# Performance work log

Hardware: AMD Instinct MI355X
Metric: run time of the kernel (lower is better)

The kernel has to match this reference:

```python
import jax, jax.numpy as jnp
import numpy as np

N, E, C = 50000, 800000, 128
NEG_SLOPE = 0.01

def leaky(v):
    return jnp.where(v >= 0, v, NEG_SLOPE * v)

def setup_inputs() -> dict:
    key = jax.random.key(0)
    ks = jax.random.split(key, 16)
    s = lambda *sh: 1.0 / np.sqrt(sh[0])
    return {
        "x": jax.random.normal(ks[0], (N, C), dtype=jnp.float32),
        "pos": jax.random.normal(ks[1], (N, 3), dtype=jnp.float32),
        "edge_index": jax.random.randint(ks[2], (2, E), 0, N, dtype=jnp.int64),
        # mlp_h: Linear(C,C) -> LeakyReLU -> Linear(C,3) -> Tanh
        "h_w1": jax.random.uniform(ks[3], (C, C), jnp.float32, -s(C), s(C)),
        "h_b1": jax.random.uniform(ks[4], (C,), jnp.float32, -s(C), s(C)),
        "h_w2": jax.random.uniform(ks[5], (C, 3), jnp.float32, -s(C), s(C)),
        "h_b2": jax.random.uniform(ks[6], (3,), jnp.float32, -s(C), s(C)),
        # mlp_f: Linear(C+3, C) -> LeakyReLU
        "f_w": jax.random.uniform(ks[7], (C + 3, C), jnp.float32, -s(C + 3), s(C + 3)),
        "f_b": jax.random.uniform(ks[8], (C,), jnp.float32, -s(C + 3), s(C + 3)),
        # mlp_g: Linear(C,C) -> LeakyReLU -> Linear(C,C)
        "g_w1": jax.random.uniform(ks[9], (C, C), jnp.float32, -s(C), s(C)),
        "g_b1": jax.random.uniform(ks[10], (C,), jnp.float32, -s(C), s(C)),
        "g_w2": jax.random.uniform(ks[11], (C, C), jnp.float32, -s(C), s(C)),
        "g_b2": jax.random.uniform(ks[12], (C,), jnp.float32, -s(C), s(C)),
    }

def reference(x, pos, edge_index, h_w1, h_b1, h_w2, h_b2, f_w, f_b,
              g_w1, g_b1, g_w2, g_b2):
    src = edge_index[0]  # j (source)
    dst = edge_index[1]  # i (target)
    # delta_i = mlp_h(x_i): [N, 3]
    delta = jnp.tanh(leaky(x @ h_w1 + h_b1) @ h_w2 + h_b2)
    # edge message: mlp_f(cat([pos_j - pos_i + delta_i, x_j]))  -> [E, C]
    rel = pos[src] - pos[dst] + delta[dst]            # [E, 3]
    msg_in = jnp.concatenate([rel, x[src]], axis=-1)  # [E, C+3]
    e = leaky(msg_in @ f_w + f_b)                     # [E, C]
    # sum-aggregate messages at target nodes
    aggr = jax.ops.segment_sum(e, dst, num_segments=N)  # [N, C]
    # out = mlp_g(aggr) + x
    out = leaky(aggr @ g_w1 + g_b1) @ g_w2 + g_b2 + x
    return out
```

## Files before the change

### kernel.cpp

```cpp
#include <hip/hip_runtime.h>
#include <hip/hip_bf16.h>
#include <math.h>


typedef __attribute__((ext_vector_type(8))) short bf16x8;
typedef __attribute__((ext_vector_type(4))) float f32x4;

#define LEAKY(v) ((v) >= 0.0f ? (v) : 0.01f * (v))

#define KMAX 512
#define S3_BATCH 8192
#define AGG_CAP 16384

static __device__ __forceinline__ unsigned short f2bf(float f) {
    unsigned u = __float_as_uint(f);
    u = (u + 0x7fffu + ((u >> 16) & 1u)) >> 16;
    return (unsigned short)u;
}

union ABu { unsigned short u[8]; bf16x8 v; };

static __device__ __forceinline__ bf16x8 cvt8(const float* __restrict__ p) {
    ABu r;
    const float4 v0 = *(const float4*)p;
    const float4 v1 = *(const float4*)(p + 4);
    r.u[0] = f2bf(v0.x); r.u[1] = f2bf(v0.y); r.u[2] = f2bf(v0.z); r.u[3] = f2bf(v0.w);
    r.u[4] = f2bf(v1.x); r.u[5] = f2bf(v1.y); r.u[6] = f2bf(v1.z); r.u[7] = f2bf(v1.w);
    return r.v;
}

static __device__ __forceinline__ bf16x8 zero_ab() {
    ABu r;
    #pragma unroll
    for (int i = 0; i < 8; ++i) r.u[i] = 0;
    return r.v;
}

static __device__ __forceinline__ void stage_weight(
    const unsigned short* __restrict__ src, unsigned short (*dst)[136], int tid)
{
    #pragma unroll
    for (int it = 0; it < 8; ++it) {
        const int c   = it * 256 + tid;
        const int row = c >> 4;
        const int col = (c & 15) * 8;
        *(uint4*)&dst[row][col] = *(const uint4*)(src + row * 128 + col);
    }
}

__global__ __launch_bounds__(128) void prep_weights(
    const float* __restrict__ h_w1, const float* __restrict__ f_w,
    const float* __restrict__ g_w1, const float* __restrict__ g_w2,
    unsigned short* __restrict__ Wht, unsigned short* __restrict__ Wft,
    unsigned short* __restrict__ G1t, unsigned short* __restrict__ G2t,
    int* __restrict__ bincnt, int* __restrict__ done)
{
    const int j = blockIdx.x;
    const int k = threadIdx.x;
    if (j == 0) {
        for (int i = k; i < KMAX; i += 128) bincnt[i] = 0;
        if (k == 0) *done = 0;
    }
    Wht[j * 128 + k] = f2bf(h_w1[(size_t)k * 128 + j]);
    Wft[j * 128 + k] = f2bf(f_w[(size_t)(3 + k) * 128 + j]);
    G1t[j * 128 + k] = f2bf(g_w1[(size_t)k * 128 + j]);
    G2t[j * 128 + k] = f2bf(g_w2[(size_t)k * 128 + j]);
}

__global__ __launch_bounds__(256) void node_pre(
    const float* __restrict__ x, const float* __restrict__ pos,
    const unsigned short* __restrict__ Wht, const float* __restrict__ h_b1,
    const float* __restrict__ h_w2, const float* __restrict__ h_b2,
    const unsigned short* __restrict__ Wft, const float* __restrict__ f_b,
    const float* __restrict__ fw3,
    float* __restrict__ deltap, unsigned short* __restrict__ Zb, int N)
{
    __shared__ unsigned short Ws[128][136];
    __shared__ float cb[128][8];

    const int tid  = threadIdx.x;
    const int lane = tid & 63;
    const int wave = tid >> 6;
    const int quad = lane >> 4;
    const int l16  = lane & 15;
    const int row0 = blockIdx.x * 64 + wave * 16;

    if (tid < 128) {
        cb[tid][0] = h_b1[tid];
        cb[tid][1] = f_b[tid];
        cb[tid][2] = h_w2[tid * 3 + 0];
        cb[tid][3] = h_w2[tid * 3 + 1];
        cb[tid][4] = h_w2[tid * 3 + 2];
        cb[tid][5] = fw3[tid];
        cb[tid][6] = fw3[128 + tid];
        cb[tid][7] = fw3[256 + tid];
    }
    stage_weight(Wht, Ws, tid);

    bf16x8 a[4];
    {
        const int row = row0 + l16;
        if (row < N) {
            const float* xp = x + (size_t)row * 128 + quad * 8;
            #pragma unroll
            for (int kc = 0; kc < 4; ++kc) a[kc] = cvt8(xp + kc * 32);
        } else {
            #pragma unroll
            for (int kc = 0; kc < 4; ++kc) a[kc] = zero_ab();
        }
    }

    float px[4], py[4], pz[4];
    #pragma unroll
    for (int reg = 0; reg < 4; ++reg) {
        const int grow = row0 + quad * 4 + reg;
        const int gr = (grow < N) ? grow : 0;
        px[reg] = pos[(size_t)gr * 3 + 0];
        py[reg] = pos[(size_t)gr * 3 + 1];
        pz[reg] = pos[(size_t)gr * 3 + 2];
    }
    __syncthreads();

    f32x4 acch[8];
    #pragma unroll
    for (int nt = 0; nt < 8; ++nt) acch[nt] = (f32x4){0.f, 0.f, 0.f, 0.f};
    #pragma unroll
    for (int nt = 0; nt < 8; ++nt) {
        const unsigned short* wp = &Ws[nt * 16 + l16][quad * 8];
        #pragma unroll
        for (int kc = 0; kc < 4; ++kc) {
            const bf16x8 b = *(const bf16x8*)(wp + kc * 32);
            acch[nt] = __builtin_amdgcn_mfma_f32_16x16x32_bf16(a[kc], b, acch[nt], 0, 0, 0);
        }
    }

    __syncthreads();
    stage_weight(Wft, Ws, tid);
    __syncthreads();

    f32x4 accf[8];
    #pragma unroll
    for (int nt = 0; nt < 8; ++nt) accf[nt] = (f32x4){0.f, 0.f, 0.f, 0.f};
    #pragma unroll
    for (int nt = 0; nt < 8; ++nt) {
        const unsigned short* wp = &Ws[nt * 16 + l16][quad * 8];
        #pragma unroll
        for (int kc = 0; kc < 4; ++kc) {
            const bf16x8 b = *(const bf16x8*)(wp + kc * 32);
            accf[nt] = __builtin_amdgcn_mfma_f32_16x16x32_bf16(a[kc], b, accf[nt], 0, 0, 0);
        }
    }

    float p[4][3];
    #pragma unroll
    for (int r = 0; r < 4; ++r) { p[r][0] = 0.f; p[r][1] = 0.f; p[r][2] = 0.f; }

    #pragma unroll
    for (int nt = 0; nt < 8; ++nt) {
        const int col = nt * 16 + l16;
        const float b1  = cb[col][0];
        const float fb  = cb[col][1];
        const float w20 = cb[col][2];
        const float w21 = cb[col][3];
        const float w22 = cb[col][4];
        const float wxc = cb[col][5];
        const float wyc = cb[col][6];
        const float wzc = cb[col][7];
        #pragma unroll
        for (int reg = 0; reg < 4; ++reg) {
            const int grow = row0 + quad * 4 + reg;
            float h = acch[nt][reg] + b1;
            h = LEAKY(h);
            p[reg][0] += h * w20;
            p[reg][1] += h * w21;
            p[reg][2] += h * w22;
            if (grow < N) {
                const float z = accf[nt][reg] + fb
                              + px[reg] * wxc + py[reg] * wyc + pz[reg] * wzc;
                Zb[(size_t)grow * 128 + col] = f2bf(z);
            }
        }
    }

    #pragma unroll
    for (int reg = 0; reg < 4; ++reg)
        #pragma unroll
        for (int c = 0; c < 3; ++c) {
            float v = p[reg][c];
            v += __shfl_down(v, 8);
            v += __shfl_down(v, 4);
            v += __shfl_down(v, 2);
            v += __shfl_down(v, 1);
            p[reg][c] = v;
        }

    if (l16 == 0) {
        #pragma unroll
        for (int reg = 0; reg < 4; ++reg) {
            const int grow = row0 + quad * 4 + reg;
            if (grow < N) {
                deltap[(size_t)grow * 3 + 0] = tanhf(p[reg][0] + h_b2[0]) - px[reg];
                deltap[(size_t)grow * 3 + 1] = tanhf(p[reg][1] + h_b2[1]) - py[reg];
                deltap[(size_t)grow * 3 + 2] = tanhf(p[reg][2] + h_b2[2]) - pz[reg];
            }
        }
    }
}

__global__ __launch_bounds__(512) void coarse_hist(
    const int* __restrict__ ei, int* __restrict__ bincnt,
    int* __restrict__ binstart, int* __restrict__ cursors,
    int* __restrict__ done, int E, int K)
{
    __shared__ int h[KMAX];
    __shared__ int s[512];
    __shared__ int lastflag;
    const int tid = threadIdx.x;
    for (int k = tid; k < K; k += 512) h[k] = 0;
    __syncthreads();
    const int stride = gridDim.x * 512;
    for (int e = blockIdx.x * 512 + tid; e < E; e += stride)
        atomicAdd(&h[ei[(size_t)E + e] >> 7], 1);
    __syncthreads();
    for (int k = tid; k < K; k += 512) {
        const int v = h[k];
        if (v) atomicAdd(&bincnt[k], v);
    }
    __threadfence();
    __syncthreads();
    if (tid == 0) lastflag = (atomicAdd(done, 1) == (int)gridDim.x - 1) ? 1 : 0;
    __syncthreads();
    if (!lastflag) return;

    const int c = (tid < K) ? atomicAdd(&bincnt[tid], 0) : 0;
    s[tid] = c;
    __syncthreads();
    for (int d = 1; d < 512; d <<= 1) {
        const int t = (tid >= d) ? s[tid - d] : 0;
        __syncthreads();
        s[tid] += t;
        __syncthreads();
    }
    if (tid < K) {
        binstart[tid] = s[tid] - c;
        cursors[tid]  = s[tid] - c;
    }
    if (tid == 0) binstart[K] = E;
}

__global__ __launch_bounds__(1024) void binsort(
    const int* __restrict__ ei, int* __restrict__ cursors,
    unsigned int* __restrict__ binned, int E, int K)
{
    __shared__ int h[KMAX];
    __shared__ int hE[KMAX];
    __shared__ int cur[KMAX];
    __shared__ int gbase[KMAX];
    __shared__ int s[512];
    __shared__ unsigned int stage[S3_BATCH];
    __shared__ unsigned short binid[S3_BATCH];

    const int tid = threadIdx.x;
    const int e0  = blockIdx.x * S3_BATCH;
    const int m   = min(S3_BATCH, E - e0);

    for (int k = tid; k < K; k += 1024) h[k] = 0;
    __syncthreads();

    #pragma unroll
    for (int j = 0; j < S3_BATCH / 1024; ++j) {
        const int i = j * 1024 + tid;
        if (i < m) atomicAdd(&h[ei[(size_t)E + e0 + i] >> 7], 1);
    }
    __syncthreads();

    int c = 0;
    if (tid < 512) {
        c = (tid < K) ? h[tid] : 0;
        s[tid] = c;
    }
    __syncthreads();
    for (int d = 1; d < 512; d <<= 1) {
        int t = 0;
        if (tid < 512 && tid >= d) t = s[tid - d];
        __syncthreads();
        if (tid < 512) s[tid] += t;
        __syncthreads();
    }
    if (tid < K) {
        const int ex = s[tid] - c;
        hE[tid]  = ex;
        cur[tid] = ex;
        gbase[tid] = c ? atomicAdd(&cursors[tid], c) : 0;
    }
    __syncthreads();

    #pragma unroll
    for (int j = 0; j < S3_BATCH / 1024; ++j) {
        const int i = j * 1024 + tid;
        if (i < m) {
            const int src = ei[e0 + i];
            const int dst = ei[(size_t)E + e0 + i];
            const int k = dst >> 7;
            const int p = atomicAdd(&cur[k], 1);
            stage[p] = (unsigned int)src | ((unsigned int)(dst & 127) << 16);
            binid[p] = (unsigned short)k;
        }
    }
    __syncthreads();

    #pragma unroll
    for (int j = 0; j < S3_BATCH / 1024; ++j) {
        const int i = j * 1024 + tid;
        if (i < m) {
            const int k = binid[i];
            binned[(size_t)gbase[k] + (i - hE[k])] = stage[i];
        }
    }
}

__global__ __launch_bounds__(1024) void bin_csr_aggregate(
    const unsigned int* __restrict__ binned, const int* __restrict__ binstart,
    const float* __restrict__ deltap,
    const unsigned short* __restrict__ Zb,
    const float* __restrict__ fw3,
    unsigned short* __restrict__ srcs_g,
    unsigned short* __restrict__ Ab,
    int N)
{
    __shared__ int h[128];
    __shared__ int s[128];
    __shared__ int cur[128];
    __shared__ unsigned short sl[AGG_CAP];

    const int tid = threadIdx.x;
    const int b   = blockIdx.x;
    const int s0  = binstart[b];
    const int s1  = binstart[b + 1];
    const int len = s1 - s0;
    const bool fits = (len <= AGG_CAP);

    if (tid < 128) h[tid] = 0;
    __syncthreads();

    for (int i = tid; i < len; i += 1024)
        atomicAdd(&h[binned[(size_t)s0 + i] >> 16], 1);
    __syncthreads();

    if (tid < 128) s[tid] = h[tid];
    __syncthreads();
    for (int d = 1; d < 128; d <<= 1) {
        int t = 0;
        if (tid < 128 && tid >= d) t = s[tid - d];
        __syncthreads();
        if (tid < 128) s[tid] += t;
        __syncthreads();
    }
    if (tid < 128) cur[tid] = s[tid] - h[tid];
    __syncthreads();

    for (int i = tid; i < len; i += 1024) {
        const unsigned int r = binned[(size_t)s0 + i];
        const int p = atomicAdd(&cur[r >> 16], 1);
        if (fits) sl[p] = (unsigned short)(r & 0xffffu);
        else      srcs_g[(size_t)s0 + p] = (unsigned short)(r & 0xffffu);
    }
    __threadfence_block();
    __syncthreads();

    const int lane    = tid & 63;
    const int wv      = tid >> 6;
    const int quarter = lane >> 4;
    const int cl      = (lane & 15) * 8;
    const int d0      = b * 128;

    for (int dl = wv; dl < 128; dl += 16) {
        const int d = d0 + dl;
        if (d >= N) continue;

        const int len_d = h[dl];
        const int start = s[dl] - h[dl];

        const float q0 = deltap[(size_t)d * 3 + 0];
        const float q1 = deltap[(size_t)d * 3 + 1];
        const float q2 = deltap[(size_t)d * 3 + 2];

        float qd[8];
        #pragma unroll
        for (int j = 0; j < 8; ++j)
            qd[j] = q0 * fw3[cl + j] + q1 * fw3[128 + cl + j] + q2 * fw3[256 + cl + j];

        float acc[8] = {0.f, 0.f, 0.f, 0.f, 0.f, 0.f, 0.f, 0.f};

        for (int chunk = 0; chunk < len_d; chunk += 64) {
            const int m = min(64, len_d - chunk);
            int idx = 0;
            if (lane < m)
                idx = fits ? (int)sl[start + chunk + lane]
                           : (int)srcs_g[(size_t)s0 + start + chunk + lane];

            int t = 0;
            #pragma unroll 4
            for (; t + 4 <= m; t += 4) {
                const int sidx = __shfl(idx, t + quarter);
                const uint4 y = *(const uint4*)(Zb + (size_t)sidx * 128 + cl);
                const float f0 = __uint_as_float((y.x & 0xffffu) << 16);
                const float f1 = __uint_as_float(y.x & 0xffff0000u);
                const float f2 = __uint_as_float((y.y & 0xffffu) << 16);
                const float f3 = __uint_as_float(y.y & 0xffff0000u);
                const float f4 = __uint_as_float((y.z & 0xffffu) << 16);
                const float f5 = __uint_as_float(y.z & 0xffff0000u);
                const float f6 = __uint_as_float((y.w & 0xffffu) << 16);
                const float f7 = __uint_as_float(y.w & 0xffff0000u);
                const float z0 = f0 + qd[0], z1 = f1 + qd[1];
                const float z2 = f2 + qd[2], z3 = f3 + qd[3];
                const float z4 = f4 + qd[4], z5 = f5 + qd[5];
                const float z6 = f6 + qd[6], z7 = f7 + qd[7];
                acc[0] += fmaxf(z0, 0.01f * z0);
                acc[1] += fmaxf(z1, 0.01f * z1);
                acc[2] += fmaxf(z2, 0.01f * z2);
                acc[3] += fmaxf(z3, 0.01f * z3);
                acc[4] += fmaxf(z4, 0.01f * z4);
                acc[5] += fmaxf(z5, 0.01f * z5);
                acc[6] += fmaxf(z6, 0.01f * z6);
                acc[7] += fmaxf(z7, 0.01f * z7);
            }
            if (t < m) {
                const int e = t + quarter;
                const int sidx = __shfl(idx, e);
                if (e < m) {
                    const uint4 y = *(const uint4*)(Zb + (size_t)sidx * 128 + cl);
                    const float f0 = __uint_as_float((y.x & 0xffffu) << 16);
                    const float f1 = __uint_as_float(y.x & 0xffff0000u);
                    const float f2 = __uint_as_float((y.y & 0xffffu) << 16);
                    const float f3 = __uint_as_float(y.y & 0xffff0000u);
                    const float f4 = __uint_as_float((y.z & 0xffffu) << 16);
                    const float f5 = __uint_as_float(y.z & 0xffff0000u);
                    const float f6 = __uint_as_float((y.w & 0xffffu) << 16);
                    const float f7 = __uint_as_float(y.w & 0xffff0000u);
                    const float z0 = f0 + qd[0], z1 = f1 + qd[1];
                    const float z2 = f2 + qd[2], z3 = f3 + qd[3];
                    const float z4 = f4 + qd[4], z5 = f5 + qd[5];
                    const float z6 = f6 + qd[6], z7 = f7 + qd[7];
                    acc[0] += fmaxf(z0, 0.01f * z0);
                    acc[1] += fmaxf(z1, 0.01f * z1);
                    acc[2] += fmaxf(z2, 0.01f * z2);
                    acc[3] += fmaxf(z3, 0.01f * z3);
                    acc[4] += fmaxf(z4, 0.01f * z4);
                    acc[5] += fmaxf(z5, 0.01f * z5);
                    acc[6] += fmaxf(z6, 0.01f * z6);
                    acc[7] += fmaxf(z7, 0.01f * z7);
                }
            }
        }

        #pragma unroll
        for (int j = 0; j < 8; ++j) {
            acc[j] += __shfl_xor(acc[j], 16);
            acc[j] += __shfl_xor(acc[j], 32);
        }
        if (quarter == 0) {
            ABu o;
            #pragma unroll
            for (int j = 0; j < 8; ++j) o.u[j] = f2bf(acc[j]);
            *(bf16x8*)(Ab + (size_t)d * 128 + cl) = o.v;
        }
    }
}

__global__ __launch_bounds__(256) void gemm_g(
    const unsigned short* __restrict__ Ab,
    const unsigned short* __restrict__ G1t, const float* __restrict__ g_b1,
    const unsigned short* __restrict__ G2t, const float* __restrict__ g_b2,
    const float* __restrict__ x,
    float* __restrict__ out, int N)
{
    __shared__ unsigned short Ws[128][136];
    __shared__ unsigned short Ts[64][136];

    const int tid  = threadIdx.x;
    const int lane = tid & 63;
    const int wave = tid >> 6;
    const int quad = lane >> 4;
    const int l16  = lane & 15;
    const int row0 = blockIdx.x * 64 + wave * 16;

    stage_weight(G1t, Ws, tid);

    bf16x8 a[4];
    {
        const int row = row0 + l16;
        if (row < N) {
            const unsigned short* ap = Ab + (size_t)row * 128 + quad * 8;
            #pragma unroll
            for (int kc = 0; kc < 4; ++kc) a[kc] = *(const bf16x8*)(ap + kc * 32);
        } else {
            #pragma unroll
            for (int kc = 0; kc < 4; ++kc) a[kc] = zero_ab();
        }
    }
    __syncthreads();

    f32x4 acc[8];
    #pragma unroll
    for (int nt = 0; nt < 8; ++nt) acc[nt] = (f32x4){0.f, 0.f, 0.f, 0.f};
    #pragma unroll
    for (int nt = 0; nt < 8; ++nt) {
        const unsigned short* wp = &Ws[nt * 16 + l16][quad * 8];
        #pragma unroll
        for (int kc = 0; kc < 4; ++kc) {
            const bf16x8 b = *(const bf16x8*)(wp + kc * 32);
            acc[nt] = __builtin_amdgcn_mfma_f32_16x16x32_bf16(a[kc], b, acc[nt], 0, 0, 0);
        }
    }

    #pragma unroll
    for (int nt = 0; nt < 8; ++nt) {
        const int col = nt * 16 + l16;
        const float b1 = g_b1[col];
        #pragma unroll
        for (int reg = 0; reg < 4; ++reg) {
            float t = acc[nt][reg] + b1;
            t = LEAKY(t);
            Ts[wave * 16 + quad * 4 + reg][col] = f2bf(t);
        }
    }
    __syncthreads();
    stage_weight(G2t, Ws, tid);
    __syncthreads();

    bf16x8 a2[4];
    {
        const unsigned short* tp = &Ts[wave * 16 + l16][quad * 8];
        #pragma unroll
        for (int kc = 0; kc < 4; ++kc) a2[kc] = *(const bf16x8*)(tp + kc * 32);
    }

    f32x4 acc2[8];
    #pragma unroll
    for (int nt = 0; nt < 8; ++nt) acc2[nt] = (f32x4){0.f, 0.f, 0.f, 0.f};
    #pragma unroll
    for (int nt = 0; nt < 8; ++nt) {
        const unsigned short* wp = &Ws[nt * 16 + l16][quad * 8];
        #pragma unroll
        for (int kc = 0; kc < 4; ++kc) {
            const bf16x8 b = *(const bf16x8*)(wp + kc * 32);
            acc2[nt] = __builtin_amdgcn_mfma_f32_16x16x32_bf16(a2[kc], b, acc2[nt], 0, 0, 0);
        }
    }

    #pragma unroll
    for (int nt = 0; nt < 8; ++nt) {
        const int col = nt * 16 + l16;
        const float b2 = g_b2[col];
        #pragma unroll
        for (int reg = 0; reg < 4; ++reg) {
            const int grow = row0 + quad * 4 + reg;
            if (grow < N)
                out[(size_t)grow * 128 + col] =
                    acc2[nt][reg] + b2 + x[(size_t)grow * 128 + col];
        }
    }
}

extern "C" void kernel_launch(void* const* d_in, const int* in_sizes, int n_in,
                              void* d_out, int out_size, void* d_ws, size_t ws_size,
                              hipStream_t stream) {
    const float* x    = (const float*)d_in[0];
    const float* pos  = (const float*)d_in[1];
    const int*   ei   = (const int*)d_in[2];
    const float* h_w1 = (const float*)d_in[3];
    const float* h_b1 = (const float*)d_in[4];
    const float* h_w2 = (const float*)d_in[5];
    const float* h_b2 = (const float*)d_in[6];
    const float* f_w  = (const float*)d_in[7];
    const float* f_b  = (const float*)d_in[8];
    const float* g_w1 = (const float*)d_in[9];
    const float* g_b1 = (const float*)d_in[10];
    const float* g_w2 = (const float*)d_in[11];
    const float* g_b2 = (const float*)d_in[12];
    float* out = (float*)d_out;

    const int N = in_sizes[0] / 128;
    const int E = in_sizes[2] / 2;
    const int K = (N + 127) >> 7;

    float* deltap         = (float*)d_ws;
    unsigned short* Zb    = (unsigned short*)(deltap + (size_t)N * 3);
    int* bincnt           = (int*)(Zb + (size_t)N * 128);
    int* binstart         = bincnt + KMAX;
    int* cursors          = binstart + (KMAX + 1);
    int* done             = cursors + KMAX;
    unsigned int* binned  = (unsigned int*)(done + 1);
    unsigned short* srcs  = (unsigned short*)(binned + E);
    unsigned short* Wht   = srcs + (((size_t)E + 1) & ~(size_t)1);
    unsigned short* Wft   = Wht + 128 * 128;
    unsigned short* G1t   = Wft + 128 * 128;
    unsigned short* G2t   = G1t + 128 * 128;
    unsigned short* Ab    = G2t + 128 * 128;

    const int tile_blocks = (N + 63) / 64;
    const int sort_blocks = (E + S3_BATCH - 1) / S3_BATCH;

    prep_weights<<<128, 128, 0, stream>>>(h_w1, f_w, g_w1, g_w2, Wht, Wft, G1t, G2t,
                                          bincnt, done);

    coarse_hist<<<128, 512, 0, stream>>>(ei, bincnt, binstart, cursors, done, E, K);

    node_pre<<<tile_blocks, 256, 0, stream>>>(x, pos, Wht, h_b1, h_w2, h_b2, Wft, f_b,
                                              f_w, deltap, Zb, N);

    binsort<<<sort_blocks, 1024, 0, stream>>>(ei, cursors, binned, E, K);

    bin_csr_aggregate<<<K, 1024, 0, stream>>>(binned, binstart, deltap, Zb, f_w,
                                              srcs, Ab, N);

    gemm_g<<<tile_blocks, 256, 0, stream>>>(Ab, G1t, g_b1, G2t, g_b2, x, out, N);
}
```

Measured before the change: 224.8 us.

## Fuse histogram into node_pre, shrink sort batches, split aggregation bins across two blocks

Merges the coarse dst histogram and prefix scan into the node preprocessing kernel by giving the first HB blocks histogram duty, which removes one launch and lets the two independent jobs run concurrently. The bin sort moves to 4096-edge batches with 512 threads, and aggregation launches two 512-thread blocks per 128-node bin, each handling one half of the destinations. The aim is more parallelism and better occupancy across the 391 bins. In exchange, every aggregation block scans the full bin's edge list and throws away half of it, and the fused kernel's shared memory layout becomes more complex.

```diff
diff --git a/kernel.cpp b/kernel.cpp
--- a/kernel.cpp
+++ b/kernel.cpp
@@ -9,7 +9,8 @@
 #define LEAKY(v) ((v) >= 0.0f ? (v) : 0.01f * (v))
 
 #define KMAX 512
-#define S3_BATCH 8192
+#define S3_BATCH 4096
+#define HB 128
 #define AGG_CAP 16384
 
 static __device__ __forceinline__ unsigned short f2bf(float f) {
@@ -67,23 +68,66 @@
     G2t[j * 128 + k] = f2bf(g_w2[(size_t)k * 128 + j]);
 }
 
-__global__ __launch_bounds__(256) void node_pre(
+__global__ __launch_bounds__(256) void fused_pre(
     const float* __restrict__ x, const float* __restrict__ pos,
     const unsigned short* __restrict__ Wht, const float* __restrict__ h_b1,
     const float* __restrict__ h_w2, const float* __restrict__ h_b2,
     const unsigned short* __restrict__ Wft, const float* __restrict__ f_b,
     const float* __restrict__ fw3,
-    float* __restrict__ deltap, unsigned short* __restrict__ Zb, int N)
+    float* __restrict__ deltap, unsigned short* __restrict__ Zb,
+    const int* __restrict__ ei, int* __restrict__ bincnt,
+    int* __restrict__ binstart, int* __restrict__ cursors,
+    int* __restrict__ done, int E, int K, int N)
 {
-    __shared__ unsigned short Ws[128][136];
-    __shared__ float cb[128][8];
-
-    const int tid  = threadIdx.x;
+    __shared__ __align__(16) unsigned char smem[34816 + 4096];
+    __shared__ int lastflag;
+
+    const int tid = threadIdx.x;
+
+    if (blockIdx.x < HB) {
+        int* h = (int*)smem;
+        int* s = (int*)(smem + 2048);
+        for (int k = tid; k < K; k += 256) h[k] = 0;
+        __syncthreads();
+        for (int e = blockIdx.x * 256 + tid; e < E; e += HB * 256)
+            atomicAdd(&h[ei[(size_t)E + e] >> 7], 1);
+        __syncthreads();
+        for (int k = tid; k < K; k += 256) {
+            const int v = h[k];
+            if (v) atomicAdd(&bincnt[k], v);
+        }
+        __threadfence();
+        __syncthreads();
+        if (tid == 0) lastflag = (atomicAdd(done, 1) == HB - 1) ? 1 : 0;
+        __syncthreads();
+        if (!lastflag) return;
+
+        const int i0 = tid * 2;
+        const int c0 = (i0 < K)     ? atomicAdd(&bincnt[i0], 0)     : 0;
+        const int c1 = (i0 + 1 < K) ? atomicAdd(&bincnt[i0 + 1], 0) : 0;
+        s[tid] = c0 + c1;
+        __syncthreads();
+        for (int d = 1; d < 256; d <<= 1) {
+            const int t = (tid >= d) ? s[tid - d] : 0;
+            __syncthreads();
+            s[tid] += t;
+            __syncthreads();
+        }
+        const int ex = s[tid] - (c0 + c1);
+        if (i0 < K)     { binstart[i0]     = ex;      cursors[i0]     = ex; }
+        if (i0 + 1 < K) { binstart[i0 + 1] = ex + c0; cursors[i0 + 1] = ex + c0; }
+        if (tid == 0) binstart[K] = E;
+        return;
+    }
+
+    unsigned short (*Ws)[136] = (unsigned short (*)[136])smem;
+    float (*cb)[8] = (float (*)[8])(smem + 34816);
+
     const int lane = tid & 63;
     const int wave = tid >> 6;
     const int quad = lane >> 4;
     const int l16  = lane & 15;
-    const int row0 = blockIdx.x * 64 + wave * 16;
+    const int row0 = (blockIdx.x - HB) * 64 + wave * 16;
 
     if (tid < 128) {
         cb[tid][0] = h_b1[tid];
@@ -207,48 +251,7 @@
     }
 }
 
-__global__ __launch_bounds__(512) void coarse_hist(
-    const int* __restrict__ ei, int* __restrict__ bincnt,
-    int* __restrict__ binstart, int* __restrict__ cursors,
-    int* __restrict__ done, int E, int K)
-{
-    __shared__ int h[KMAX];
-    __shared__ int s[512];
-    __shared__ int lastflag;
-    const int tid = threadIdx.x;
-    for (int k = tid; k < K; k += 512) h[k] = 0;
-    __syncthreads();
-    const int stride = gridDim.x * 512;
-    for (int e = blockIdx.x * 512 + tid; e < E; e += stride)
-        atomicAdd(&h[ei[(size_t)E + e] >> 7], 1);
-    __syncthreads();
-    for (int k = tid; k < K; k += 512) {
-        const int v = h[k];
-        if (v) atomicAdd(&bincnt[k], v);
-    }
-    __threadfence();
-    __syncthreads();
-    if (tid == 0) lastflag = (atomicAdd(done, 1) == (int)gridDim.x - 1) ? 1 : 0;
-    __syncthreads();
-    if (!lastflag) return;
-
-    const int c = (tid < K) ? atomicAdd(&bincnt[tid], 0) : 0;
-    s[tid] = c;
-    __syncthreads();
-    for (int d = 1; d < 512; d <<= 1) {
-        const int t = (tid >= d) ? s[tid - d] : 0;
-        __syncthreads();
-        s[tid] += t;
-        __syncthreads();
-    }
-    if (tid < K) {
-        binstart[tid] = s[tid] - c;
-        cursors[tid]  = s[tid] - c;
-    }
-    if (tid == 0) binstart[K] = E;
-}
-
-__global__ __launch_bounds__(1024) void binsort(
+__global__ __launch_bounds__(512) void binsort(
     const int* __restrict__ ei, int* __restrict__ cursors,
     unsigned int* __restrict__ binned, int E, int K)
 {
@@ -264,27 +267,23 @@
     const int e0  = blockIdx.x * S3_BATCH;
     const int m   = min(S3_BATCH, E - e0);
 
-    for (int k = tid; k < K; k += 1024) h[k] = 0;
-    __syncthreads();
-
-    #pragma unroll
-    for (int j = 0; j < S3_BATCH / 1024; ++j) {
-        const int i = j * 1024 + tid;
+    for (int k = tid; k < K; k += 512) h[k] = 0;
+    __syncthreads();
+
+    #pragma unroll
+    for (int j = 0; j < S3_BATCH / 512; ++j) {
+        const int i = j * 512 + tid;
         if (i < m) atomicAdd(&h[ei[(size_t)E + e0 + i] >> 7], 1);
     }
     __syncthreads();
 
-    int c = 0;
-    if (tid < 512) {
-        c = (tid < K) ? h[tid] : 0;
-        s[tid] = c;
-    }
+    const int c = (tid < K) ? h[tid] : 0;
+    s[tid] = c;
     __syncthreads();
     for (int d = 1; d < 512; d <<= 1) {
-        int t = 0;
-        if (tid < 512 && tid >= d) t = s[tid - d];
-        __syncthreads();
-        if (tid < 512) s[tid] += t;
+        const int t = (tid >= d) ? s[tid - d] : 0;
+        __syncthreads();
+        s[tid] += t;
         __syncthreads();
     }
     if (tid < K) {
@@ -296,8 +295,8 @@
     __syncthreads();
 
     #pragma unroll
-    for (int j = 0; j < S3_BATCH / 1024; ++j) {
-        const int i = j * 1024 + tid;
+    for (int j = 0; j < S3_BATCH / 512; ++j) {
+        const int i = j * 512 + tid;
         if (i < m) {
             const int src = ei[e0 + i];
             const int dst = ei[(size_t)E + e0 + i];
@@ -310,8 +309,8 @@
     __syncthreads();
 
     #pragma unroll
-    for (int j = 0; j < S3_BATCH / 1024; ++j) {
-        const int i = j * 1024 + tid;
+    for (int j = 0; j < S3_BATCH / 512; ++j) {
+        const int i = j * 512 + tid;
         if (i < m) {
             const int k = binid[i];
             binned[(size_t)gbase[k] + (i - hE[k])] = stage[i];
@@ -319,7 +318,7 @@
     }
 }
 
-__global__ __launch_bounds__(1024) void bin_csr_aggregate(
+__global__ __launch_bounds__(512) void bin_csr_aggregate(
     const unsigned int* __restrict__ binned, const int* __restrict__ binstart,
     const float* __restrict__ deltap,
     const unsigned short* __restrict__ Zb,
@@ -328,42 +327,51 @@
     unsigned short* __restrict__ Ab,
     int N)
 {
-    __shared__ int h[128];
-    __shared__ int s[128];
-    __shared__ int cur[128];
+    __shared__ int h[64];
+    __shared__ int s[64];
+    __shared__ int cur[64];
     __shared__ unsigned short sl[AGG_CAP];
 
-    const int tid = threadIdx.x;
-    const int b   = blockIdx.x;
-    const int s0  = binstart[b];
-    const int s1  = binstart[b + 1];
-    const int len = s1 - s0;
-    const bool fits = (len <= AGG_CAP);
-
-    if (tid < 128) h[tid] = 0;
-    __syncthreads();
-
-    for (int i = tid; i < len; i += 1024)
-        atomicAdd(&h[binned[(size_t)s0 + i] >> 16], 1);
-    __syncthreads();
-
-    if (tid < 128) s[tid] = h[tid];
-    __syncthreads();
-    for (int d = 1; d < 128; d <<= 1) {
+    const int tid  = threadIdx.x;
+    const int bin  = blockIdx.x >> 1;
+    const int half = blockIdx.x & 1;
+    const int s0   = binstart[bin];
+    const int s1   = binstart[bin + 1];
+    const int len  = s1 - s0;
+
+    if (tid < 64) h[tid] = 0;
+    __syncthreads();
+
+    for (int i = tid; i < len; i += 512) {
+        const int dl16 = binned[(size_t)s0 + i] >> 16;
+        if ((dl16 >> 6) == half) atomicAdd(&h[dl16 & 63], 1);
+    }
+    __syncthreads();
+
+    if (tid < 64) s[tid] = h[tid];
+    __syncthreads();
+    for (int d = 1; d < 64; d <<= 1) {
         int t = 0;
-        if (tid < 128 && tid >= d) t = s[tid - d];
-        __syncthreads();
-        if (tid < 128) s[tid] += t;
-        __syncthreads();
-    }
-    if (tid < 128) cur[tid] = s[tid] - h[tid];
-    __syncthreads();
-
-    for (int i = tid; i < len; i += 1024) {
+        if (tid < 64 && tid >= d) t = s[tid - d];
+        __syncthreads();
+        if (tid < 64) s[tid] += t;
+        __syncthreads();
+    }
+    if (tid < 64) cur[tid] = s[tid] - h[tid];
+    __syncthreads();
+
+    const int own   = s[63];
+    const bool fits = (own <= AGG_CAP);
+    const int gb    = half ? (s1 - own) : s0;
+
+    for (int i = tid; i < len; i += 512) {
         const unsigned int r = binned[(size_t)s0 + i];
-        const int p = atomicAdd(&cur[r >> 16], 1);
-        if (fits) sl[p] = (unsigned short)(r & 0xffffu);
-        else      srcs_g[(size_t)s0 + p] = (unsigned short)(r & 0xffffu);
+        const int dl16 = r >> 16;
+        if ((dl16 >> 6) == half) {
+            const int p = atomicAdd(&cur[dl16 & 63], 1);
+            if (fits) sl[p] = (unsigned short)(r & 0xffffu);
+            else      srcs_g[(size_t)gb + p] = (unsigned short)(r & 0xffffu);
+        }
     }
     __threadfence_block();
     __syncthreads();
@@ -372,9 +380,9 @@
     const int wv      = tid >> 6;
     const int quarter = lane >> 4;
     const int cl      = (lane & 15) * 8;
-    const int d0      = b * 128;
-
-    for (int dl = wv; dl < 128; dl += 16) {
+    const int d0      = bin * 128 + half * 64;
+
+    for (int dl = wv; dl < 64; dl += 8) {
         const int d = d0 + dl;
         if (d >= N) continue;
 
@@ -397,7 +405,7 @@
             int idx = 0;
             if (lane < m)
                 idx = fits ? (int)sl[start + chunk + lane]
-                           : (int)srcs_g[(size_t)s0 + start + chunk + lane];
+                           : (int)srcs_g[(size_t)gb + start + chunk + lane];
 
             int t = 0;
             #pragma unroll 4
@@ -605,15 +613,14 @@
     prep_weights<<<128, 128, 0, stream>>>(h_w1, f_w, g_w1, g_w2, Wht, Wft, G1t, G2t,
                                           bincnt, done);
 
-    coarse_hist<<<128, 512, 0, stream>>>(ei, bincnt, binstart, cursors, done, E, K);
-
-    node_pre<<<tile_blocks, 256, 0, stream>>>(x, pos, Wht, h_b1, h_w2, h_b2, Wft, f_b,
-                                              f_w, deltap, Zb, N);
-
-    binsort<<<sort_blocks, 1024, 0, stream>>>(ei, cursors, binned, E, K);
-
-    bin_csr_aggregate<<<K, 1024, 0, stream>>>(binned, binstart, deltap, Zb, f_w,
-                                              srcs, Ab, N);
+    fused_pre<<<HB + tile_blocks, 256, 0, stream>>>(
+        x, pos, Wht, h_b1, h_w2, h_b2, Wft, f_b, f_w,
+        deltap, Zb, ei, bincnt, binstart, cursors, done, E, K, N);
+
+    binsort<<<sort_blocks, 512, 0, stream>>>(ei, cursors, binned, E, K);
+
+    bin_csr_aggregate<<<K * 2, 512, 0, stream>>>(binned, binstart, deltap, Zb, f_w,
+                                                 srcs, Ab, N);
 
     gemm_g<<<tile_blocks, 256, 0, stream>>>(Ab, G1t, g_b1, G2t, g_b2, x, out, N);
 }
```

New measurement: 222.4 us. Within noise of the previous version (-1.1%).
